# Performance work log

Measured on AMD Instinct MI355X. Metric: run time of the kernel, lower is better.

Reference implementation:

```python
import jax, jax.numpy as jnp
import numpy as np

N = 100000
E = 1600000
IN_C = 256
HID = 256
OUT_C = 10
G = 64  # number of graphs in batch


def setup_inputs() -> dict:
    key = jax.random.key(0)
    k1, k2, k3, k4, k5, k6, k7 = jax.random.split(key, 7)
    x = jax.random.normal(k1, (N, IN_C), dtype=jnp.float32)
    edge_index = jax.random.randint(k2, (2, E), 0, N, dtype=jnp.int64)
    batch = jnp.sort(jax.random.randint(k3, (N,), 0, G, dtype=jnp.int64))
    # GCNConv weight (glorot-ish) and bias
    W1 = jax.random.normal(k4, (IN_C, HID), dtype=jnp.float32) / np.sqrt(IN_C)
    b1 = jnp.zeros((HID,), dtype=jnp.float32)
    # final Linear
    W2 = jax.random.normal(k5, (HID, OUT_C), dtype=jnp.float32) / np.sqrt(HID)
    b2 = jax.random.normal(k6, (OUT_C,), dtype=jnp.float32) * 0.01
    return {"x": x, "edge_index": edge_index, "batch": batch,
            "W1": W1, "b1": b1, "W2": W2, "b2": b2}


def reference(x, edge_index, batch, W1, b1, W2, b2):
    # ---- GCNConv(in_channels, hidden_dim), add_self_loops=True, symmetric norm ----
    src = edge_index[0]
    dst = edge_index[1]
    loop = jnp.arange(N, dtype=src.dtype)
    src = jnp.concatenate([src, loop])  # [E+N]
    dst = jnp.concatenate([dst, loop])
    # degree on destination nodes (incl. self-loops) -> >= 1 everywhere
    deg = jax.ops.segment_sum(jnp.ones_like(dst, dtype=x.dtype), dst, num_segments=N)
    dinv = jax.lax.rsqrt(deg)  # deg >= 1, safe
    h = x @ W1  # linear transform first (PyG GCNConv order)
    norm = dinv[src] * dinv[dst]  # [E+N]
    msgs = h[src] * norm[:, None]  # gather + scale
    agg = jax.ops.segment_sum(msgs, dst, num_segments=N) + b1  # scatter-add + bias
    # ---- relu; dropout is identity in eval mode ----
    hrelu = jax.nn.relu(agg)
    # ---- global_mean_pool over batch ids ----
    sums = jax.ops.segment_sum(hrelu, batch, num_segments=G)
    counts = jax.ops.segment_sum(jnp.ones((N,), dtype=x.dtype), batch, num_segments=G)
    pooled = sums / jnp.maximum(counts, 1.0)[:, None]  # [G, HID]
    # ---- final linear ----
    return pooled @ W2 + b2
```

## Files before the change

kernel.cpp:

```cpp
#include <hip/hip_runtime.h>

#define NN 100000
#define EE 1600000
#define C 256
#define OUTC 10
#define NG 64

#define NBK 391
#define CHUNK 16384
#define NBLK1 ((EE + CHUNK - 1) / CHUNK)
#define PADSLACK 2048

#define NODES_PER_GROUP 8
#define NODES_PER_BLOCK 32

typedef __bf16 bf16x8 __attribute__((ext_vector_type(8)));
typedef float f32x4 __attribute__((ext_vector_type(4)));
typedef float f32x2 __attribute__((ext_vector_type(2)));

__device__ __forceinline__ ushort f2bf(float f) {
    unsigned u = __float_as_uint(f);
    return (ushort)((u + 0x7fffu + ((u >> 16) & 1u)) >> 16);
}
__device__ __forceinline__ bf16x8 as_bf16x8(uint4 v) {
    union { uint4 u; bf16x8 b; } c; c.u = v; return c.b;
}

__device__ __forceinline__ uchar f2fp8(float f) {
    return (uchar)(__builtin_amdgcn_cvt_pk_fp8_f32(f, 0.f, 0, false) & 0xff);
}
__device__ __forceinline__ void acc_fp8x4(float4& s, unsigned v) {
    f32x2 lo = __builtin_amdgcn_cvt_pk_f32_fp8(v, false);
    f32x2 hi = __builtin_amdgcn_cvt_pk_f32_fp8(v, true);
    s.x += lo[0]; s.y += lo[1]; s.z += hi[0]; s.w += hi[1];
}

__global__ __launch_bounds__(1024) void count_kernel(const int* __restrict__ batch,
                                                     float* __restrict__ cnt) {
    __shared__ int h[NG];
    if (threadIdx.x < NG) h[threadIdx.x] = 0;
    __syncthreads();
    int i = blockIdx.x * blockDim.x + threadIdx.x;
    if (i < NN) atomicAdd(&h[batch[i]], 1);
    __syncthreads();
    if (threadIdx.x < NG) {
        int v = h[threadIdx.x];
        if (v > 0) atomicAdd(&cnt[threadIdx.x], (float)v);
    }
}

__global__ __launch_bounds__(256) void bucket_hist_kernel(const int* __restrict__ ei,
                                                          int* __restrict__ bhist) {
    __shared__ int h[NBK];
    for (int t = threadIdx.x; t < NBK; t += 256) h[t] = 0;
    __syncthreads();
    const int base = blockIdx.x * CHUNK;
    const int end = min(base + CHUNK, EE);
    for (int e = base + threadIdx.x; e < end; e += 256)
        atomicAdd(&h[ei[EE + e] >> 8], 1);
    __syncthreads();
    for (int t = threadIdx.x; t < NBK; t += 256)
        if (h[t]) atomicAdd(&bhist[t], h[t]);
}

__global__ __launch_bounds__(512) void bucket_scan_kernel(const int* __restrict__ bhist,
                                                          int* __restrict__ bbase,
                                                          int* __restrict__ bcur) {
    __shared__ int sc[512];
    const int t = threadIdx.x;
    int v = (t < NBK) ? bhist[t] : 0;
    sc[t] = v;
    __syncthreads();
    for (int off = 1; off < 512; off <<= 1) {
        int tmp = (t >= off) ? sc[t - off] : 0;
        __syncthreads();
        sc[t] += tmp;
        __syncthreads();
    }
    int excl = sc[t] - v;
    if (t < NBK) { bbase[t] = excl; bcur[t] = excl; }
    if (t == 0) bbase[NBK] = sc[511];
}

__global__ __launch_bounds__(256) void bucket_scatter_kernel(const int* __restrict__ ei,
                                                             int* __restrict__ bcur,
                                                             unsigned* __restrict__ bmaj) {
    __shared__ int h[NBK];
    for (int t = threadIdx.x; t < NBK; t += 256) h[t] = 0;
    __syncthreads();
    const int base = blockIdx.x * CHUNK;
    const int end = min(base + CHUNK, EE);
    for (int e = base + threadIdx.x; e < end; e += 256)
        atomicAdd(&h[ei[EE + e] >> 8], 1);
    __syncthreads();
    for (int t = threadIdx.x; t < NBK; t += 256) {
        int c = h[t];
        h[t] = c ? atomicAdd(&bcur[t], c) : 0;
    }
    __syncthreads();
    for (int e = base + threadIdx.x; e < end; e += 256) {
        int d = ei[EE + e];
        int s = ei[e];
        int b = d >> 8;
        int p = atomicAdd(&h[b], 1);
        bmaj[p] = (unsigned)s | ((unsigned)(d & 255) << 17);
    }
}

__global__ __launch_bounds__(256) void bucket_csr_kernel(const unsigned* __restrict__ bmaj,
                                                         const int* __restrict__ bbase,
                                                         int* __restrict__ rowend,
                                                         float* __restrict__ dinv,
                                                         int* __restrict__ csrcol) {
    __shared__ int h[256];
    __shared__ int sc[256];
    __shared__ int cur[256];
    const int b = blockIdx.x;
    const int t = threadIdx.x;
    const int e0 = bbase[b], e1 = bbase[b + 1];
    const int region0 = e0 + b * PADSLACK;
    h[t] = 0;
    __syncthreads();
    for (int e = e0 + t; e < e1; e += 256)
        atomicAdd(&h[bmaj[e] >> 17], 1);
    __syncthreads();
    int deg = h[t];
    int pd = (deg + 7) & ~7;
    sc[t] = pd;
    __syncthreads();
    for (int off = 1; off < 256; off <<= 1) {
        int tmp = (t >= off) ? sc[t - off] : 0;
        __syncthreads();
        sc[t] += tmp;
        __syncthreads();
    }
    int pstart = region0 + sc[t] - pd;
    int node = b * 256 + t;
    if (node < NN) {
        rowend[node] = pstart + pd;
        dinv[node] = rsqrtf((float)deg + 1.0f);
        for (int j = deg; j < pd; j++) csrcol[pstart + j] = NN;
    }
    cur[t] = pstart;
    __syncthreads();
    for (int e = e0 + t; e < e1; e += 256) {
        unsigned v = bmaj[e];
        int p = atomicAdd(&cur[v >> 17], 1);
        csrcol[p] = (int)(v & 0x1FFFFu);
    }
}

__global__ __launch_bounds__(256) void w1pack_kernel(const float* __restrict__ W1,
                                                     ushort* __restrict__ w1f,
                                                     unsigned* __restrict__ gz) {
    int t = blockIdx.x * 256 + threadIdx.x;
    if (blockIdx.x == 0 && threadIdx.x < 64) gz[threadIdx.x] = 0;
    int k = t >> 8, n = t & 255;
    int kb = k >> 5, q = (k >> 3) & 3, j = k & 7;
    int nt = n >> 4, ln = (n & 15) + q * 16;
    w1f[(size_t)(((kb * 16 + nt) * 64) + ln) * 8 + j] = f2bf(W1[t]);
}

__global__ __launch_bounds__(256) void gemm_mfma_kernel(const float* __restrict__ x,
                                                        const ushort* __restrict__ w1f,
                                                        const float* __restrict__ dinv,
                                                        uchar* __restrict__ g) {
    const int lane = threadIdx.x & 63;
    const int wid = threadIdx.x >> 6;
    const int wave = blockIdx.x * 4 + wid;
    const int r0 = wave * 32;
    if (r0 >= NN) return;
    const int mrow = lane & 15;
    const int q = lane >> 4;

    f32x4 acc[2][16];
    #pragma unroll
    for (int mt = 0; mt < 2; mt++)
        #pragma unroll
        for (int nt = 0; nt < 16; nt++)
            acc[mt][nt] = (f32x4){0.f, 0.f, 0.f, 0.f};

    const float* xp0 = x + (size_t)(r0 + mrow) * C + q * 8;
    const float* xp1 = xp0 + (size_t)16 * C;
    const ushort* bp = w1f + (size_t)lane * 8;

    #pragma unroll 1
    for (int kb = 0; kb < 8; kb++) {
        const int ko = kb * 32;
        float4 a0lo = *(const float4*)(xp0 + ko);
        float4 a0hi = *(const float4*)(xp0 + ko + 4);
        float4 a1lo = *(const float4*)(xp1 + ko);
        float4 a1hi = *(const float4*)(xp1 + ko + 4);
        bf16x8 a0, a1;
        a0[0] = (__bf16)a0lo.x; a0[1] = (__bf16)a0lo.y;
        a0[2] = (__bf16)a0lo.z; a0[3] = (__bf16)a0lo.w;
        a0[4] = (__bf16)a0hi.x; a0[5] = (__bf16)a0hi.y;
        a0[6] = (__bf16)a0hi.z; a0[7] = (__bf16)a0hi.w;
        a1[0] = (__bf16)a1lo.x; a1[1] = (__bf16)a1lo.y;
        a1[2] = (__bf16)a1lo.z; a1[3] = (__bf16)a1lo.w;
        a1[4] = (__bf16)a1hi.x; a1[5] = (__bf16)a1hi.y;
        a1[6] = (__bf16)a1hi.z; a1[7] = (__bf16)a1hi.w;

        const ushort* bkb = bp + (size_t)kb * 16 * 512;
        #pragma unroll
        for (int nt = 0; nt < 16; nt++) {
            bf16x8 bb = as_bf16x8(*(const uint4*)(bkb + (size_t)nt * 512));
            acc[0][nt] = __builtin_amdgcn_mfma_f32_16x16x32_bf16(a0, bb, acc[0][nt], 0, 0, 0);
            acc[1][nt] = __builtin_amdgcn_mfma_f32_16x16x32_bf16(a1, bb, acc[1][nt], 0, 0, 0);
        }
    }

    #pragma unroll
    for (int mt = 0; mt < 2; mt++) {
        #pragma unroll
        for (int r = 0; r < 4; r++) {
            int row = r0 + mt * 16 + q * 4 + r;
            float dv = dinv[row];
            uchar* gp = g + (size_t)row * C + mrow;
            #pragma unroll
            for (int nt = 0; nt < 16; nt++)
                gp[nt * 16] = f2fp8(acc[mt][nt][r] * dv);
        }
    }
}

__global__ __launch_bounds__(256) void agg_pool_kernel(const unsigned* __restrict__ g32,
                                                       const int* __restrict__ rowend,
                                                       const int* __restrict__ csrcol,
                                                       const int* __restrict__ bbase,
                                                       const float* __restrict__ dinv,
                                                       const float* __restrict__ b1,
                                                       const int* __restrict__ batch,
                                                       float* __restrict__ sums) {
    const int lane = threadIdx.x & 63;
    const int wid = threadIdx.x >> 6;
    const int c4 = lane * 4;
    const int nodeA = blockIdx.x * NODES_PER_BLOCK + wid * NODES_PER_GROUP;
    const float4 bv = *(const float4*)&b1[c4];

    int rprev;
    if ((nodeA & 255) == 0) {
        int b = nodeA >> 8;
        rprev = bbase[b] + b * PADSLACK;
    } else {
        rprev = rowend[nodeA - 1];
    }

    float4 pool = make_float4(0.f, 0.f, 0.f, 0.f);
    int curb = -1;
    #pragma unroll 1
    for (int i = nodeA; i < nodeA + NODES_PER_GROUP; i++) {
        int r1 = rowend[i];
        int r0 = rprev;
        rprev = r1;
        int bi = batch[i];
        if (bi != curb) {
            if (curb >= 0) {
                atomicAdd(&sums[curb * C + c4 + 0], pool.x);
                atomicAdd(&sums[curb * C + c4 + 1], pool.y);
                atomicAdd(&sums[curb * C + c4 + 2], pool.z);
                atomicAdd(&sums[curb * C + c4 + 3], pool.w);
            }
            curb = bi;
            pool = make_float4(0.f, 0.f, 0.f, 0.f);
        }
        float4 s = make_float4(0.f, 0.f, 0.f, 0.f);
        acc_fp8x4(s, g32[(size_t)i * 64 + lane]);
        #pragma unroll 1
        for (int e = r0; e < r1; e += 8) {
            int i0 = csrcol[e],     i1 = csrcol[e + 1];
            int i2 = csrcol[e + 2], i3 = csrcol[e + 3];
            int i4 = csrcol[e + 4], i5 = csrcol[e + 5];
            int i6 = csrcol[e + 6], i7 = csrcol[e + 7];
            unsigned v0 = g32[(size_t)i0 * 64 + lane];
            unsigned v1 = g32[(size_t)i1 * 64 + lane];
            unsigned v2 = g32[(size_t)i2 * 64 + lane];
            unsigned v3 = g32[(size_t)i3 * 64 + lane];
            unsigned v4 = g32[(size_t)i4 * 64 + lane];
            unsigned v5 = g32[(size_t)i5 * 64 + lane];
            unsigned v6 = g32[(size_t)i6 * 64 + lane];
            unsigned v7 = g32[(size_t)i7 * 64 + lane];
            acc_fp8x4(s, v0); acc_fp8x4(s, v1); acc_fp8x4(s, v2); acc_fp8x4(s, v3);
            acc_fp8x4(s, v4); acc_fp8x4(s, v5); acc_fp8x4(s, v6); acc_fp8x4(s, v7);
        }
        float dv = dinv[i];
        pool.x += fmaxf(fmaf(dv, s.x, bv.x), 0.f);
        pool.y += fmaxf(fmaf(dv, s.y, bv.y), 0.f);
        pool.z += fmaxf(fmaf(dv, s.z, bv.z), 0.f);
        pool.w += fmaxf(fmaf(dv, s.w, bv.w), 0.f);
    }
    if (curb >= 0) {
        atomicAdd(&sums[curb * C + c4 + 0], pool.x);
        atomicAdd(&sums[curb * C + c4 + 1], pool.y);
        atomicAdd(&sums[curb * C + c4 + 2], pool.z);
        atomicAdd(&sums[curb * C + c4 + 3], pool.w);
    }
}

__global__ __launch_bounds__(256) void final_kernel(const float* __restrict__ sums,
                                                    const float* __restrict__ cnt,
                                                    const float* __restrict__ W2,
                                                    const float* __restrict__ b2,
                                                    float* __restrict__ out) {
    __shared__ float p[C];
    int gi = blockIdx.x;
    float cdiv = fmaxf(cnt[gi], 1.0f);
    p[threadIdx.x] = sums[gi * C + threadIdx.x] / cdiv;
    __syncthreads();
    if (threadIdx.x < OUTC) {
        float acc = b2[threadIdx.x];
        for (int k = 0; k < C; k++) acc += p[k] * W2[k * OUTC + threadIdx.x];
        out[gi * OUTC + threadIdx.x] = acc;
    }
}

extern "C" void kernel_launch(void* const* d_in, const int* in_sizes, int n_in,
                              void* d_out, int out_size, void* d_ws, size_t ws_size,
                              hipStream_t stream) {
    const float* x     = (const float*)d_in[0];
    const int*   ei    = (const int*)d_in[1];
    const int*   batch = (const int*)d_in[2];
    const float* W1    = (const float*)d_in[3];
    const float* b1    = (const float*)d_in[4];
    const float* W2    = (const float*)d_in[5];
    const float* b2    = (const float*)d_in[6];
    float* out = (float*)d_out;

    char* w = (char*)d_ws;
    size_t off = 0;
    auto carve = [&](size_t bytes) {
        void* p = w + off;
        off = (off + bytes + 255) & ~(size_t)255;
        return p;
    };
    uchar*    g        = (uchar*)   carve((size_t)(NN + 1) * C);
    int*      rowend   = (int*)     carve((size_t)NN * 4);
    float*    dinv     = (float*)   carve((size_t)NN * 4);
    int*      csrcol   = (int*)     carve((size_t)(EE + NBK * PADSLACK) * 4);
    unsigned* bmaj     = (unsigned*)carve((size_t)EE * 4);
    int*      bbase    = (int*)     carve((size_t)(NBK + 1) * 4);
    int*      bcur     = (int*)     carve((size_t)NBK * 4);
    ushort*   w1f      = (ushort*)  carve((size_t)C * C * 2);
    int*      bhist    = (int*)     carve((size_t)NBK * 4);
    float*    sums     = (float*)   carve((size_t)NG * C * 4);
    float*    cnt      = (float*)   carve((size_t)NG * 4);
    size_t zero_bytes = (size_t)((char*)cnt + (size_t)NG * 4 - (char*)bhist);

    hipMemsetAsync(bhist, 0, zero_bytes, stream);

    bucket_hist_kernel<<<NBLK1, 256, 0, stream>>>(ei, bhist);
    bucket_scan_kernel<<<1, 512, 0, stream>>>(bhist, bbase, bcur);
    bucket_scatter_kernel<<<NBLK1, 256, 0, stream>>>(ei, bcur, bmaj);
    bucket_csr_kernel<<<NBK, 256, 0, stream>>>(bmaj, bbase, rowend, dinv, csrcol);
    count_kernel<<<(NN + 1023) / 1024, 1024, 0, stream>>>(batch, cnt);
    w1pack_kernel<<<C * C / 256, 256, 0, stream>>>(W1, w1f, (unsigned*)(g + (size_t)NN * C));
    gemm_mfma_kernel<<<(NN / 32 + 3) / 4, 256, 0, stream>>>(x, w1f, dinv, g);
    agg_pool_kernel<<<NN / NODES_PER_BLOCK, 256, 0, stream>>>(
        (const unsigned*)g, rowend, csrcol, bbase, dinv, b1, batch, sums);
    final_kernel<<<NG, 256, 0, stream>>>(sums, cnt, W2, b2, out);
}
```

Baseline: 425.7 us.

## Permute fp8 channel layout for vector stores, fold self-loop into CSR, vectorize index loads

The GEMM epilogue now packs 16 fp8 values per row into one 16-byte store instead of 16 scattered byte stores. This permutes the channel order in g, so the bias and W2 lookups go through a logical-channel remap. The self-loop is written as the first CSR entry of each row, and the CSR region is aligned so column indices can be read as int4. The bucketing CHUNK is reduced to give the histogram and scatter kernels more blocks, at the cost of extra padding and more atomics.

```diff
diff --git a/kernel.cpp b/kernel.cpp
--- a/kernel.cpp
+++ b/kernel.cpp
@@ -7,9 +7,9 @@
 #define NG 64
 
 #define NBK 391
-#define CHUNK 16384
+#define CHUNK 2048
 #define NBLK1 ((EE + CHUNK - 1) / CHUNK)
-#define PADSLACK 2048
+#define PADSLACK 2304
 
 #define NODES_PER_GROUP 8
 #define NODES_PER_BLOCK 32
@@ -18,6 +18,10 @@
 typedef float f32x4 __attribute__((ext_vector_type(4)));
 typedef float f32x2 __attribute__((ext_vector_type(2)));
 
+__device__ __forceinline__ int chan_logical(int p) {
+    return ((p & 15) << 4) | (p >> 4);
+}
+
 __device__ __forceinline__ ushort f2bf(float f) {
     unsigned u = __float_as_uint(f);
     return (ushort)((u + 0x7fffu + ((u >> 16) & 1u)) >> 16);
@@ -26,9 +30,6 @@
     union { uint4 u; bf16x8 b; } c; c.u = v; return c.b;
 }
 
-__device__ __forceinline__ uchar f2fp8(float f) {
-    return (uchar)(__builtin_amdgcn_cvt_pk_fp8_f32(f, 0.f, 0, false) & 0xff);
-}
 __device__ __forceinline__ void acc_fp8x4(float4& s, unsigned v) {
     f32x2 lo = __builtin_amdgcn_cvt_pk_f32_fp8(v, false);
     f32x2 hi = __builtin_amdgcn_cvt_pk_f32_fp8(v, true);
@@ -118,14 +119,15 @@
     const int b = blockIdx.x;
     const int t = threadIdx.x;
     const int e0 = bbase[b], e1 = bbase[b + 1];
-    const int region0 = e0 + b * PADSLACK;
+    const int region0 = ((e0 + 7) & ~7) + b * PADSLACK;
     h[t] = 0;
     __syncthreads();
     for (int e = e0 + t; e < e1; e += 256)
         atomicAdd(&h[bmaj[e] >> 17], 1);
     __syncthreads();
     int deg = h[t];
-    int pd = (deg + 7) & ~7;
+    int node = b * 256 + t;
+    int pd = (node < NN) ? ((deg + 8) & ~7) : 0;
     sc[t] = pd;
     __syncthreads();
     for (int off = 1; off < 256; off <<= 1) {
@@ -135,13 +137,13 @@
         __syncthreads();
     }
     int pstart = region0 + sc[t] - pd;
-    int node = b * 256 + t;
     if (node < NN) {
         rowend[node] = pstart + pd;
         dinv[node] = rsqrtf((float)deg + 1.0f);
-        for (int j = deg; j < pd; j++) csrcol[pstart + j] = NN;
-    }
-    cur[t] = pstart;
+        csrcol[pstart] = node;
+        for (int j = deg + 1; j < pd; j++) csrcol[pstart + j] = NN;
+    }
+    cur[t] = pstart + 1;
     __syncthreads();
     for (int e = e0 + t; e < e1; e += 256) {
         unsigned v = bmaj[e];
@@ -216,10 +218,17 @@
         for (int r = 0; r < 4; r++) {
             int row = r0 + mt * 16 + q * 4 + r;
             float dv = dinv[row];
-            uchar* gp = g + (size_t)row * C + mrow;
-            #pragma unroll
-            for (int nt = 0; nt < 16; nt++)
-                gp[nt * 16] = f2fp8(acc[mt][nt][r] * dv);
+            uint4 dw;
+            unsigned t0, t1, t2, t3;
+            t0 = __builtin_amdgcn_cvt_pk_fp8_f32(acc[mt][0][r] * dv,  acc[mt][1][r] * dv,  0,  false);
+            dw.x = __builtin_amdgcn_cvt_pk_fp8_f32(acc[mt][2][r] * dv,  acc[mt][3][r] * dv,  t0, true);
+            t1 = __builtin_amdgcn_cvt_pk_fp8_f32(acc[mt][4][r] * dv,  acc[mt][5][r] * dv,  0,  false);
+            dw.y = __builtin_amdgcn_cvt_pk_fp8_f32(acc[mt][6][r] * dv,  acc[mt][7][r] * dv,  t1, true);
+            t2 = __builtin_amdgcn_cvt_pk_fp8_f32(acc[mt][8][r] * dv,  acc[mt][9][r] * dv,  0,  false);
+            dw.z = __builtin_amdgcn_cvt_pk_fp8_f32(acc[mt][10][r] * dv, acc[mt][11][r] * dv, t2, true);
+            t3 = __builtin_amdgcn_cvt_pk_fp8_f32(acc[mt][12][r] * dv, acc[mt][13][r] * dv, 0,  false);
+            dw.w = __builtin_amdgcn_cvt_pk_fp8_f32(acc[mt][14][r] * dv, acc[mt][15][r] * dv, t3, true);
+            *(uint4*)(g + (size_t)row * C + mrow * 16) = dw;
         }
     }
 }
@@ -236,12 +245,17 @@
     const int wid = threadIdx.x >> 6;
     const int c4 = lane * 4;
     const int nodeA = blockIdx.x * NODES_PER_BLOCK + wid * NODES_PER_GROUP;
-    const float4 bv = *(const float4*)&b1[c4];
+    float4 bv;
+    bv.x = b1[chan_logical(c4 + 0)];
+    bv.y = b1[chan_logical(c4 + 1)];
+    bv.z = b1[chan_logical(c4 + 2)];
+    bv.w = b1[chan_logical(c4 + 3)];
+    const unsigned* gp = g32 + lane;
 
     int rprev;
     if ((nodeA & 255) == 0) {
         int b = nodeA >> 8;
-        rprev = bbase[b] + b * PADSLACK;
+        rprev = ((bbase[b] + 7) & ~7) + b * PADSLACK;
     } else {
         rprev = rowend[nodeA - 1];
     }
@@ -265,21 +279,18 @@
             pool = make_float4(0.f, 0.f, 0.f, 0.f);
         }
         float4 s = make_float4(0.f, 0.f, 0.f, 0.f);
-        acc_fp8x4(s, g32[(size_t)i * 64 + lane]);
         #pragma unroll 1
         for (int e = r0; e < r1; e += 8) {
-            int i0 = csrcol[e],     i1 = csrcol[e + 1];
-            int i2 = csrcol[e + 2], i3 = csrcol[e + 3];
-            int i4 = csrcol[e + 4], i5 = csrcol[e + 5];
-            int i6 = csrcol[e + 6], i7 = csrcol[e + 7];
-            unsigned v0 = g32[(size_t)i0 * 64 + lane];
-            unsigned v1 = g32[(size_t)i1 * 64 + lane];
-            unsigned v2 = g32[(size_t)i2 * 64 + lane];
-            unsigned v3 = g32[(size_t)i3 * 64 + lane];
-            unsigned v4 = g32[(size_t)i4 * 64 + lane];
-            unsigned v5 = g32[(size_t)i5 * 64 + lane];
-            unsigned v6 = g32[(size_t)i6 * 64 + lane];
-            unsigned v7 = g32[(size_t)i7 * 64 + lane];
+            int4 iv0 = *(const int4*)(csrcol + e);
+            int4 iv1 = *(const int4*)(csrcol + e + 4);
+            unsigned v0 = gp[(size_t)iv0.x * 64];
+            unsigned v1 = gp[(size_t)iv0.y * 64];
+            unsigned v2 = gp[(size_t)iv0.z * 64];
+            unsigned v3 = gp[(size_t)iv0.w * 64];
+            unsigned v4 = gp[(size_t)iv1.x * 64];
+            unsigned v5 = gp[(size_t)iv1.y * 64];
+            unsigned v6 = gp[(size_t)iv1.z * 64];
+            unsigned v7 = gp[(size_t)iv1.w * 64];
             acc_fp8x4(s, v0); acc_fp8x4(s, v1); acc_fp8x4(s, v2); acc_fp8x4(s, v3);
             acc_fp8x4(s, v4); acc_fp8x4(s, v5); acc_fp8x4(s, v6); acc_fp8x4(s, v7);
         }
@@ -309,7 +320,8 @@
     __syncthreads();
     if (threadIdx.x < OUTC) {
         float acc = b2[threadIdx.x];
-        for (int k = 0; k < C; k++) acc += p[k] * W2[k * OUTC + threadIdx.x];
+        for (int k = 0; k < C; k++)
+            acc += p[k] * W2[chan_logical(k) * OUTC + threadIdx.x];
         out[gi * OUTC + threadIdx.x] = acc;
     }
 }
@@ -336,7 +348,7 @@
     uchar*    g        = (uchar*)   carve((size_t)(NN + 1) * C);
     int*      rowend   = (int*)     carve((size_t)NN * 4);
     float*    dinv     = (float*)   carve((size_t)NN * 4);
-    int*      csrcol   = (int*)     carve((size_t)(EE + NBK * PADSLACK) * 4);
+    int*      csrcol   = (int*)     carve((size_t)(EE + (size_t)NBK * PADSLACK + 128) * 4);
     unsigned* bmaj     = (unsigned*)carve((size_t)EE * 4);
     int*      bbase    = (int*)     carve((size_t)(NBK + 1) * 4);
     int*      bcur     = (int*)     carve((size_t)NBK * 4);
```

After: 415.3 us. 2.4% less time.
